# Kernel optimization log

Measured on AMD Instinct MI355X. Metric: run time of the kernel, lower is better.

Reference implementation:

```python
import jax, jax.numpy as jnp
import numpy as np

N = 50000      # nodes
E = 1600000    # edges (nnz of A)
D_IN = 512
D_H = 512
D_OUT = 40
L = 3
LN_EPS = 1e-5
BN_EPS = 1e-5


def setup_inputs() -> dict:
    key = jax.random.key(0)
    ks = jax.random.split(key, 10)
    x = jax.random.normal(ks[0], (N, D_IN), dtype=jnp.float32)
    edge_src = jax.random.randint(ks[1], (E,), 0, N, dtype=jnp.int32)
    edge_dst = jax.random.randint(ks[2], (E,), 0, N, dtype=jnp.int32)
    s = 1.0 / np.sqrt(D_IN)
    W_in = (jax.random.normal(ks[3], (D_IN, D_H), dtype=jnp.float32) * s)
    b_in = jnp.zeros((D_H,), jnp.float32)
    ln_g = jnp.ones((D_H,), jnp.float32)
    ln_b = jnp.zeros((D_H,), jnp.float32)
    cW1 = (jax.random.normal(ks[4], (D_H, D_H), dtype=jnp.float32) * s)
    cb1 = jnp.zeros((D_H,), jnp.float32)
    bn_g = 1.0 + 0.1 * jax.random.normal(ks[5], (D_H,), dtype=jnp.float32)
    bn_b = 0.1 * jax.random.normal(ks[6], (D_H,), dtype=jnp.float32)
    bn_mean = jnp.zeros((D_H,), jnp.float32)   # eval-mode running stats
    bn_var = jnp.ones((D_H,), jnp.float32)
    cW2 = (jax.random.normal(ks[7], (D_H, D_OUT), dtype=jnp.float32) * s)
    cb2 = jnp.zeros((D_OUT,), jnp.float32)
    return dict(x=x, edge_src=edge_src, edge_dst=edge_dst, W_in=W_in, b_in=b_in,
                ln_g=ln_g, ln_b=ln_b, cW1=cW1, cb1=cb1, bn_g=bn_g, bn_b=bn_b,
                bn_mean=bn_mean, bn_var=bn_var, cW2=cW2, cb2=cb2)


def _agg_angle(h, edge_src, edge_dst, dinv):
    # diag(D^-1/2 A D^-1/2 @ CosSim^T)[i] = sum_{(i,j) in A} dinv_i dinv_j cos(h_i,h_j)
    nrm = jnp.sqrt(jnp.sum(h * h, axis=1, keepdims=True))  # torch.norm p=2
    hn = h / (nrm + 1e-4)
    cos_e = jnp.clip(jnp.sum(hn[edge_src] * hn[edge_dst], axis=1), -1.0, 1.0)  # [E]
    w_e = dinv[edge_src] * dinv[edge_dst] * cos_e
    return jax.ops.segment_sum(w_e, edge_src, num_segments=N)  # [N]


def _forward(x, edge_src, edge_dst, W_in, b_in, ln_g, ln_b, cW1, cb1,
             bn_g, bn_b, bn_mean, bn_var, cW2, cb2):
    h = jax.nn.relu(x @ W_in + b_in)
    mu = jnp.mean(h, axis=-1, keepdims=True)
    var = jnp.var(h, axis=-1, keepdims=True)
    h = (h - mu) / jnp.sqrt(var + LN_EPS) * ln_g + ln_b   # LayerNorm
    # dropout: eval mode -> identity
    # degree normalization (adjacency values are all 1.0); constant across layers
    deg = jax.ops.segment_sum(jnp.ones((E,), h.dtype), edge_src, num_segments=N)
    dinv = jnp.where(deg > 0, deg ** -0.5, 0.0)
    for _ in range(L):
        ang = _agg_angle(h, edge_src, edge_dst, dinv)  # [N]
        c, s = jnp.cos(ang), jnp.sin(ang)
        r0 = c * h[:, 0] - s * h[:, 1]   # 2x2 Givens rotation on first two dims
        r1 = s * h[:, 0] + c * h[:, 1]
        h = jnp.concatenate([jnp.stack([r0, r1], axis=1), h[:, 2:]], axis=1)
    # classifier: Linear -> ReLU -> BatchNorm1d (eval) -> Linear
    z = jax.nn.relu(h @ cW1 + cb1)
    z = (z - bn_mean) / jnp.sqrt(bn_var + BN_EPS) * bn_g + bn_b
    logits = z @ cW2 + cb2
    return jax.nn.log_softmax(logits, axis=1)


def reference(x, edge_src, edge_dst, W_in, b_in, ln_g, ln_b, cW1, cb1,
              bn_g, bn_b, bn_mean, bn_var, cW2, cb2):
    return _forward(x, edge_src, edge_dst, W_in, b_in, ln_g, ln_b, cW1, cb1,
                    bn_g, bn_b, bn_mean, bn_var, cW2, cb2)
```

## Files before the change

kernel.cpp:

```cpp
#include <hip/hip_runtime.h>
#include <hip/hip_bf16.h>
#include <math.h>

typedef unsigned short u16;
typedef unsigned int u32;

#define N_NODES 50000
#define N_EDGES 1600000
#define DIM     512
#define DOUT    40
#define MPAD    50048
#define QROW    256
#define NBKT    196
#define NB1     256
#define CHUNK   6250

typedef __bf16 bf16x8 __attribute__((ext_vector_type(8)));
typedef float  f32x4  __attribute__((ext_vector_type(4)));

__device__ inline u16 f2bf(float f) {
    union { float f; u32 u; } v; v.f = f;
    u32 u = v.u;
    u32 r = u + 0x7fffu + ((u >> 16) & 1u);
    return (u16)(r >> 16);
}
__device__ inline float2 bfpair(u32 u) {
    float2 r;
    union { u32 i; float f; } lo, hi;
    lo.i = u << 16; hi.i = u & 0xffff0000u;
    r.x = lo.f; r.y = hi.f; return r;
}
__device__ inline float wave_sum(float v) {
    #pragma unroll
    for (int o = 32; o > 0; o >>= 1) v += __shfl_xor(v, o);
    return v;
}
__device__ inline float wave_max(float v) {
    #pragma unroll
    for (int o = 32; o > 0; o >>= 1) v = fmaxf(v, __shfl_xor(v, o));
    return v;
}
__device__ inline int wave_sum_i(int v) {
    #pragma unroll
    for (int o = 32; o > 0; o >>= 1) v += __shfl_xor(v, o);
    return v;
}
#if __has_builtin(__builtin_amdgcn_sdot8)
__device__ inline int dot8(int a, int b, int c) {
    return __builtin_amdgcn_sdot8(a, b, c, false);
}
#else
__device__ inline int dot8(int a, int b, int c) {
    #pragma unroll
    for (int j = 0; j < 8; ++j) {
        int av = ((int)((u32)a << (28 - 4 * j))) >> 28;
        int bv = ((int)((u32)b << (28 - 4 * j))) >> 28;
        c += av * bv;
    }
    return c;
}
#endif
__device__ inline void gload16(const void* g, void* l) {
    __builtin_amdgcn_global_load_lds((const __attribute__((address_space(1))) u32*)g,
                                     (__attribute__((address_space(3))) u32*)l, 16, 0, 0);
}
__device__ inline int block_incl_scan(int v, int tid) {
    int lane = tid & 63, w = tid >> 6;
    #pragma unroll
    for (int o = 1; o < 64; o <<= 1) {
        int t = __shfl_up(v, o);
        if (lane >= o) v += t;
    }
    __shared__ int wsum[4];
    if (lane == 63) wsum[w] = v;
    __syncthreads();
    if (w > 0) v += wsum[0];
    if (w > 1) v += wsum[1];
    if (w > 2) v += wsum[2];
    return v;
}

__global__ __launch_bounds__(256) void k_conv_x(const float* __restrict__ x,
                                                u16* __restrict__ xb) {
    long idx = (long)blockIdx.x * 256 + threadIdx.x;
    long base = idx * 4;
    if (base >= (long)MPAD * DIM) return;
    long row = base >> 9;
    float4 v;
    if (row < N_NODES) v = *(const float4*)(x + base);
    else { v.x = v.y = v.z = v.w = 0.f; }
    ushort4 o;
    o.x = f2bf(v.x); o.y = f2bf(v.y); o.z = f2bf(v.z); o.w = f2bf(v.w);
    *(ushort4*)(xb + base) = o;
}

__global__ __launch_bounds__(256) void k_transpose2(const float* __restrict__ W0,
                                                    const float* __restrict__ W1,
                                                    u16* __restrict__ T0,
                                                    u16* __restrict__ T1) {
    const float* W = blockIdx.z ? W1 : W0;
    u16* T = blockIdx.z ? T1 : T0;
    int n = blockIdx.x * 16 + threadIdx.x;
    int k = blockIdx.y * 16 + threadIdx.y;
    T[(long)n * 512 + k] = f2bf(W[(long)k * 512 + n]);
}
__global__ __launch_bounds__(256) void k_prep_w2(const float* __restrict__ cW2,
                                                 u16* __restrict__ W2b) {
    int idx = blockIdx.x * 256 + threadIdx.x;
    if (idx >= 48 * DIM) return;
    int n = idx >> 9;
    int k = idx & 511;
    float v = (n < DOUT) ? cW2[(long)k * DOUT + n] : 0.f;
    W2b[idx] = f2bf(v);
}

__global__ __launch_bounds__(256) void k_ms_count(const int* __restrict__ esrc,
                                                  int* __restrict__ C) {
    __shared__ int bcnt[NBKT];
    int tid = threadIdx.x, blk = blockIdx.x;
    if (tid < NBKT) bcnt[tid] = 0;
    __syncthreads();
    int e0 = blk * CHUNK, e1 = e0 + CHUNK;
    for (int e = e0 + tid; e < e1; e += 256)
        atomicAdd(&bcnt[esrc[e] >> 8], 1);
    __syncthreads();
    if (tid < NBKT) C[tid * NB1 + blk] = bcnt[tid];
}
__global__ __launch_bounds__(256) void k_ms_scan_partial(const int* __restrict__ C,
                                                         int* __restrict__ psum2) {
    int v = C[blockIdx.x * 256 + threadIdx.x];
    int t = wave_sum_i(v);
    __shared__ int ws[4];
    int lane = threadIdx.x & 63, w = threadIdx.x >> 6;
    if (lane == 0) ws[w] = t;
    __syncthreads();
    if (threadIdx.x == 0) psum2[blockIdx.x] = ws[0] + ws[1] + ws[2] + ws[3];
}
__global__ __launch_bounds__(256) void k_ms_scan_base(const int* __restrict__ psum2,
                                                      int* __restrict__ pb2) {
    int tid = threadIdx.x;
    int v = (tid < NBKT) ? psum2[tid] : 0;
    int incl = block_incl_scan(v, tid);
    if (tid < NBKT) pb2[tid] = incl - v;
}
__global__ __launch_bounds__(256) void k_ms_scan_add(const int* __restrict__ C,
                                                     const int* __restrict__ pb2,
                                                     int* __restrict__ O) {
    int idx = blockIdx.x * 256 + threadIdx.x;
    int v = C[idx];
    int incl = block_incl_scan(v, threadIdx.x);
    O[idx] = pb2[blockIdx.x] + incl - v;
}
__global__ __launch_bounds__(256) void k_ms_scatter(const int* __restrict__ esrc,
                                                    const int* __restrict__ edst,
                                                    const int* __restrict__ O,
                                                    uint2* __restrict__ tmp) {
    __shared__ int cur[NBKT];
    int tid = threadIdx.x, blk = blockIdx.x;
    if (tid < NBKT) cur[tid] = O[tid * NB1 + blk];
    __syncthreads();
    int e0 = blk * CHUNK, e1 = e0 + CHUNK;
    for (int e = e0 + tid; e < e1; e += 256) {
        int s = esrc[e], d = edst[e];
        int pos = atomicAdd(&cur[s >> 8], 1);
        uint2 pr; pr.x = (u32)s; pr.y = (u32)d;
        tmp[pos] = pr;
    }
}
__global__ __launch_bounds__(256) void k_bucket(const int* __restrict__ Om,
                                                const uint2* __restrict__ tmp,
                                                int* __restrict__ rowptr,
                                                float* __restrict__ dinv,
                                                int* __restrict__ edst_s) {
    __shared__ int cnt[256];
    __shared__ int curs[256];
    int tid = threadIdx.x, b = blockIdx.x;
    int base = b * 256;
    int start = Om[b * NB1];
    int end = (b == NBKT - 1) ? N_EDGES : Om[(b + 1) * NB1];
    cnt[tid] = 0;
    __syncthreads();
    for (int p = start + tid; p < end; p += 256)
        atomicAdd(&cnt[(int)tmp[p].x - base], 1);
    __syncthreads();
    int c = cnt[tid];
    int incl = block_incl_scan(c, tid);
    int excl = incl - c;
    int node = base + tid;
    if (node < N_NODES) {
        rowptr[node] = start + excl;
        dinv[node] = (c > 0) ? (1.f / sqrtf((float)c)) : 0.f;
    }
    if (b == NBKT - 1 && tid == 0) rowptr[N_NODES] = N_EDGES;
    curs[tid] = start + excl;
    __syncthreads();
    for (int p = start + tid; p < end; p += 256) {
        uint2 pr = tmp[p];
        int pos = atomicAdd(&curs[(int)pr.x - base], 1);
        edst_s[pos] = (int)pr.y;
    }
}

template<int EPI>
__global__ __launch_bounds__(256) void k_gemm(const u16* __restrict__ A,
                                              const u16* __restrict__ Bt,
                                              u16* __restrict__ outB,
                                              const float* __restrict__ bias,
                                              const float* __restrict__ bn_g,
                                              const float* __restrict__ bn_b,
                                              const float* __restrict__ bn_mean,
                                              const float* __restrict__ bn_var) {
    __shared__ u16 lds[2 * 128 * 64];
    char* ldsA = (char*)lds;
    char* ldsB = (char*)lds + 16384;

    const int bid = blockIdx.x;
    const int xcd = bid & 7;
    const int j = bid >> 3;
    const int tm = xcd * 49 + (j >> 2);
    const int tn = j & 3;
    if (tm >= MPAD / 128) return;

    const int tid = threadIdx.x;
    const int l = tid & 63, wid = tid >> 6;
    const int wr = wid >> 1, wc = wid & 1;
    const int lm = l & 15, lk = l >> 4;

    const int srow = tid >> 3;
    const int kq   = tid & 7;

    f32x4 acc[4][4] = {};

    for (int kt = 0; kt < 8; ++kt) {
        const int k0 = kt * 64;
        #pragma unroll
        for (int r = 0; r < 4; ++r) {
            int row = r * 32 + srow;
            int kc = (kq ^ (row & 7)) * 8;
            const u16* ga = A + ((long)tm * 128 + row) * DIM + k0 + kc;
            const u16* gb = Bt + ((long)tn * 128 + row) * DIM + k0 + kc;
            char* la = ldsA + r * 4096 + wid * 1024;
            char* lb = ldsB + r * 4096 + wid * 1024;
            gload16(ga, la);
            gload16(gb, lb);
        }
        __syncthreads();
        #pragma unroll
        for (int kk = 0; kk < 2; ++kk) {
            bf16x8 af[4], bfr[4];
            #pragma unroll
            for (int m = 0; m < 4; ++m) {
                int ar = wr * 64 + m * 16 + lm;
                af[m] = *(const bf16x8*)(ldsA + ar * 128 + ((kk * 64 + lk * 16) ^ ((ar & 7) << 4)));
            }
            #pragma unroll
            for (int n = 0; n < 4; ++n) {
                int br = wc * 64 + n * 16 + lm;
                bfr[n] = *(const bf16x8*)(ldsB + br * 128 + ((kk * 64 + lk * 16) ^ ((br & 7) << 4)));
            }
            #pragma unroll
            for (int m = 0; m < 4; ++m)
                #pragma unroll
                for (int n = 0; n < 4; ++n)
                    acc[m][n] = __builtin_amdgcn_mfma_f32_16x16x32_bf16(af[m], bfr[n], acc[m][n], 0, 0, 0);
        }
        __syncthreads();
    }

    #pragma unroll
    for (int n = 0; n < 4; ++n) {
        int col = tn * 128 + wc * 64 + n * 16 + lm;
        float bc = bias[col];
        float scale = 0.f, shift = 0.f;
        if (EPI == 1) {
            scale = bn_g[col] / sqrtf(bn_var[col] + 1e-5f);
            shift = bn_b[col] - bn_mean[col] * scale;
        }
        #pragma unroll
        for (int m = 0; m < 4; ++m) {
            f32x4 v = acc[m][n];
            #pragma unroll
            for (int r = 0; r < 4; ++r) {
                long row = (long)tm * 128 + wr * 64 + m * 16 + lk * 4 + r;
                float val = fmaxf(v[r] + bc, 0.f);
                if (EPI == 1) val = val * scale + shift;
                outB[row * DIM + col] = f2bf(val);
            }
        }
    }
}

__global__ __launch_bounds__(256) void k_ln(u16* __restrict__ hb,
                                            char* __restrict__ hq,
                                            float* __restrict__ stepr,
                                            const float* __restrict__ g,
                                            const float* __restrict__ b,
                                            float* __restrict__ a0,
                                            float* __restrict__ a1,
                                            float* __restrict__ inv_nrm) {
    int row = blockIdx.x * 4 + (threadIdx.x >> 6);
    int l = threadIdx.x & 63;
    u16* prow = hb + (long)row * DIM + l * 8;
    if (row >= N_NODES) {
        if (row < MPAD) { uint4 z; z.x = z.y = z.z = z.w = 0u; *(uint4*)prow = z; }
        return;
    }
    uint4 v = *(const uint4*)prow;
    float x[8];
    { float2 p;
      p = bfpair(v.x); x[0] = p.x; x[1] = p.y;
      p = bfpair(v.y); x[2] = p.x; x[3] = p.y;
      p = bfpair(v.z); x[4] = p.x; x[5] = p.y;
      p = bfpair(v.w); x[6] = p.x; x[7] = p.y; }
    float s = 0.f, sq = 0.f;
    #pragma unroll
    for (int j = 0; j < 8; ++j) { s += x[j]; sq += x[j] * x[j]; }
    #pragma unroll
    for (int o = 32; o > 0; o >>= 1) { s += __shfl_xor(s, o); sq += __shfl_xor(sq, o); }
    float mean = s * (1.f / DIM);
    float var = sq * (1.f / DIM) - mean * mean;
    float rstd = 1.f / sqrtf(var + 1e-5f);
    float y[8];
    #pragma unroll
    for (int j = 0; j < 8; ++j) {
        int c = l * 8 + j;
        y[j] = (x[j] - mean) * rstd * g[c] + b[c];
    }
    float s2 = 0.f;
    #pragma unroll
    for (int j = 0; j < 8; ++j) s2 += y[j] * y[j];
    s2 = wave_sum(s2);
    float nrm = sqrtf(s2);
    float inv = 1.f / (nrm + 1e-4f);
    ushort4 oh;
    oh.x = f2bf(y[0]); oh.y = f2bf(y[1]); oh.z = f2bf(y[2]); oh.w = f2bf(y[3]);
    *(ushort4*)prow = oh;
    oh.x = f2bf(y[4]); oh.y = f2bf(y[5]); oh.z = f2bf(y[6]); oh.w = f2bf(y[7]);
    *(ushort4*)(prow + 4) = oh;
    float nv[8];
    float mx = 0.f;
    #pragma unroll
    for (int j = 0; j < 8; ++j) { nv[j] = y[j] * inv; mx = fmaxf(mx, fabsf(nv[j])); }
    mx = wave_max(mx);
    float qs = (mx > 0.f) ? (7.f / mx) : 0.f;
    if (l == 0) { nv[0] = 0.f; nv[1] = 0.f; }
    u32 w = 0;
    #pragma unroll
    for (int j = 0; j < 8; ++j) {
        int q = (int)rintf(nv[j] * qs);
        w |= ((u32)(q & 0xF)) << (4 * j);
    }
    *(u32*)(hq + (long)row * QROW + l * 4) = w;
    if (l == 0) {
        stepr[row] = (mx > 0.f) ? (mx * (1.f / 7.f)) : 0.f;
        a0[row] = y[0]; a1[row] = y[1]; inv_nrm[row] = inv;
    }
}

__global__ __launch_bounds__(256) void k_edge_dot(const int* __restrict__ rowptr,
                                                  const int* __restrict__ edst_s,
                                                  const char* __restrict__ hq,
                                                  const float* __restrict__ stepr,
                                                  float* __restrict__ rest) {
    int node = blockIdx.x * 4 + (threadIdx.x >> 6);
    if (node >= N_NODES) return;
    int l = threadIdx.x & 63;
    int le = l & 7;
    int eg = l >> 3;
    int p0 = rowptr[node], p1 = rowptr[node + 1];
    if (p0 == p1) return;
    const int4* srow = (const int4*)(hq + (long)node * QROW);
    int4 s0 = srow[le * 2], s1 = srow[le * 2 + 1];
    float ss = stepr[node];
    #pragma unroll 2
    for (int base = p0; base < p1; base += 8) {
        int p = base + eg;
        bool ok = p < p1;
        int d = ok ? edst_s[p] : 0;
        const int4* drow = (const int4*)(hq + (long)d * QROW);
        int4 d0 = drow[le * 2], d1 = drow[le * 2 + 1];
        int acc = 0;
        acc = dot8(s0.x, d0.x, acc); acc = dot8(s0.y, d0.y, acc);
        acc = dot8(s0.z, d0.z, acc); acc = dot8(s0.w, d0.w, acc);
        acc = dot8(s1.x, d1.x, acc); acc = dot8(s1.y, d1.y, acc);
        acc = dot8(s1.z, d1.z, acc); acc = dot8(s1.w, d1.w, acc);
        acc += __shfl_xor(acc, 4);
        acc += __shfl_xor(acc, 2);
        acc += __shfl_xor(acc, 1);
        if (ok && le == 0) rest[p] = ss * stepr[d] * (float)acc;
    }
}

template<int WRITE_HB>
__global__ __launch_bounds__(256) void k_layer(const int* __restrict__ rowptr,
                                               const int* __restrict__ edst_s,
                                               const float* __restrict__ rest,
                                               const float* __restrict__ a0i,
                                               const float* __restrict__ a1i,
                                               const float* __restrict__ invn,
                                               const float* __restrict__ dinv,
                                               float* __restrict__ a0o,
                                               float* __restrict__ a1o,
                                               u16* __restrict__ hb) {
    int node = blockIdx.x * 4 + (threadIdx.x >> 6);
    if (node >= N_NODES) return;
    int l = threadIdx.x & 63;
    int p0 = rowptr[node], p1 = rowptr[node + 1];
    float x = a0i[node], y = a1i[node];
    float si = invn[node];
    float sa0 = x * si, sa1 = y * si;
    float accum = 0.f;
    for (int p = p0 + l; p < p1; p += 64) {
        int d = edst_s[p];
        float c = rest[p] + (sa0 * a0i[d] + sa1 * a1i[d]) * invn[d];
        c = fminf(1.f, fmaxf(-1.f, c));
        accum += dinv[d] * c;
    }
    accum = wave_sum(accum);
    if (l == 0) {
        float ang = dinv[node] * accum;
        float sn, cs;
        sincosf(ang, &sn, &cs);
        float r0 = cs * x - sn * y;
        float r1 = sn * x + cs * y;
        a0o[node] = r0;
        a1o[node] = r1;
        if (WRITE_HB) {
            hb[(long)node * DIM + 0] = f2bf(r0);
            hb[(long)node * DIM + 1] = f2bf(r1);
        }
    }
}

__global__ __launch_bounds__(256) void k_final(const u16* __restrict__ zb,
                                               const u16* __restrict__ W2b,
                                               const float* __restrict__ cb2,
                                               float* __restrict__ out) {
    __shared__ char ldsB[48 * 1024];
    const int tid = threadIdx.x;
    #pragma unroll
    for (int i = 0; i < 12; ++i) {
        int unit = i * 256 + tid;
        int byte = unit * 16;
        int row = byte >> 10;
        int colb = byte & 1023;
        uint4 v = *(const uint4*)((const char*)W2b + byte);
        *(uint4*)(ldsB + row * 1024 + (colb ^ ((row & 7) << 4))) = v;
    }
    __syncthreads();

    const int l = tid & 63, wid = tid >> 6;
    const int lm = l & 15, lk = l >> 4;
    const long m0 = (long)blockIdx.x * 128 + wid * 32;

    f32x4 acc[2][3] = {};
    for (int kt = 0; kt < 16; ++kt) {
        const int k0 = kt * 32;
        bf16x8 af[2], bfr[3];
        #pragma unroll
        for (int m = 0; m < 2; ++m)
            af[m] = *(const bf16x8*)(zb + (m0 + m * 16 + lm) * DIM + k0 + lk * 8);
        #pragma unroll
        for (int n = 0; n < 3; ++n) {
            int br = n * 16 + lm;
            bfr[n] = *(const bf16x8*)(ldsB + br * 1024 + ((k0 * 2 + lk * 16) ^ ((br & 7) << 4)));
        }
        #pragma unroll
        for (int m = 0; m < 2; ++m)
            #pragma unroll
            for (int n = 0; n < 3; ++n)
                acc[m][n] = __builtin_amdgcn_mfma_f32_16x16x32_bf16(af[m], bfr[n], acc[m][n], 0, 0, 0);
    }

    float bc[3];
    #pragma unroll
    for (int n = 0; n < 3; ++n) {
        int col = n * 16 + lm;
        bc[n] = (col < DOUT) ? cb2[col] : 0.f;
    }

    #pragma unroll
    for (int m = 0; m < 2; ++m) {
        #pragma unroll
        for (int r = 0; r < 4; ++r) {
            long row = m0 + m * 16 + lk * 4 + r;
            float v[3];
            float mv = -1e30f;
            #pragma unroll
            for (int n = 0; n < 3; ++n) {
                int col = n * 16 + lm;
                float t = (col < DOUT) ? (acc[m][n][r] + bc[n]) : -1e30f;
                v[n] = t;
                mv = fmaxf(mv, t);
            }
            #pragma unroll
            for (int o = 8; o > 0; o >>= 1) mv = fmaxf(mv, __shfl_xor(mv, o));
            float es = 0.f;
            #pragma unroll
            for (int n = 0; n < 3; ++n) {
                int col = n * 16 + lm;
                if (col < DOUT) es += expf(v[n] - mv);
            }
            #pragma unroll
            for (int o = 8; o > 0; o >>= 1) es += __shfl_xor(es, o);
            float lse = logf(es);
            if (row < N_NODES) {
                #pragma unroll
                for (int n = 0; n < 3; ++n) {
                    int col = n * 16 + lm;
                    if (col < DOUT) out[row * DOUT + col] = v[n] - mv - lse;
                }
            }
        }
    }
}

extern "C" void kernel_launch(void* const* d_in, const int* in_sizes, int n_in,
                              void* d_out, int out_size, void* d_ws, size_t ws_size,
                              hipStream_t stream) {
    const float* x       = (const float*)d_in[0];
    const int*   esrc    = (const int*)d_in[1];
    const int*   edst    = (const int*)d_in[2];
    const float* W_in    = (const float*)d_in[3];
    const float* b_in    = (const float*)d_in[4];
    const float* ln_g    = (const float*)d_in[5];
    const float* ln_b    = (const float*)d_in[6];
    const float* cW1     = (const float*)d_in[7];
    const float* cb1     = (const float*)d_in[8];
    const float* bn_g    = (const float*)d_in[9];
    const float* bn_b    = (const float*)d_in[10];
    const float* bn_mean = (const float*)d_in[11];
    const float* bn_var  = (const float*)d_in[12];
    const float* cW2     = (const float*)d_in[13];
    const float* cb2     = (const float*)d_in[14];
    float* out = (float*)d_out;

    char* ws = (char*)d_ws;
    size_t off = 0;
    auto take = [&](size_t bytes) -> char* {
        char* p = ws + off;
        off = (off + bytes + 255) & ~(size_t)255;
        return p;
    };
    u16*   xb     = (u16*)take((size_t)MPAD * DIM * 2);
    u16*   hb     = (u16*)take((size_t)MPAD * DIM * 2);
    char*  hq     = (char*)take((size_t)N_NODES * QROW);
    float* stepr  = (float*)take((size_t)N_NODES * 4);
    u16*   WtIn   = (u16*)take((size_t)512 * 512 * 2);
    u16*   W1t    = (u16*)take((size_t)512 * 512 * 2);
    u16*   W2b    = (u16*)take((size_t)48 * 512 * 2);
    float* dinv   = (float*)take((size_t)N_NODES * 4);
    float* a0A    = (float*)take((size_t)N_NODES * 4);
    float* a1A    = (float*)take((size_t)N_NODES * 4);
    float* a0B    = (float*)take((size_t)N_NODES * 4);
    float* a1B    = (float*)take((size_t)N_NODES * 4);
    float* invn   = (float*)take((size_t)N_NODES * 4);
    float* rest   = (float*)take((size_t)N_EDGES * 4);
    int*   rowptr = (int*)take((size_t)(N_NODES + 1) * 4);
    int*   edst_s = (int*)take((size_t)N_EDGES * 4);
    uint2* tmp    = (uint2*)take((size_t)N_EDGES * 8);
    int*   Cm     = (int*)take((size_t)NBKT * NB1 * 4);
    int*   Om     = (int*)take((size_t)NBKT * NB1 * 4);
    int*   psum2  = (int*)take((size_t)NBKT * 4);
    int*   pb2    = (int*)take((size_t)NBKT * 4);
    u16*   zb     = xb;

    k_conv_x<<<(MPAD * DIM / 4 + 255) / 256, 256, 0, stream>>>(x, xb);
    k_transpose2<<<dim3(32, 32, 2), dim3(16, 16), 0, stream>>>(W_in, cW1, WtIn, W1t);
    k_prep_w2<<<(48 * DIM + 255) / 256, 256, 0, stream>>>(cW2, W2b);

    k_ms_count<<<NB1, 256, 0, stream>>>(esrc, Cm);
    k_ms_scan_partial<<<NBKT, 256, 0, stream>>>(Cm, psum2);
    k_ms_scan_base<<<1, 256, 0, stream>>>(psum2, pb2);
    k_ms_scan_add<<<NBKT, 256, 0, stream>>>(Cm, pb2, Om);
    k_ms_scatter<<<NB1, 256, 0, stream>>>(esrc, edst, Om, tmp);
    k_bucket<<<NBKT, 256, 0, stream>>>(Om, tmp, rowptr, dinv, edst_s);

    k_gemm<0><<<1568, 256, 0, stream>>>(xb, WtIn, hb, b_in,
                                        nullptr, nullptr, nullptr, nullptr);
    k_ln<<<MPAD / 4, 256, 0, stream>>>(hb, hq, stepr, ln_g, ln_b, a0A, a1A, invn);
    k_edge_dot<<<(N_NODES + 3) / 4, 256, 0, stream>>>(rowptr, edst_s, hq, stepr, rest);

    k_layer<0><<<(N_NODES + 3) / 4, 256, 0, stream>>>(rowptr, edst_s, rest,
                                                      a0A, a1A, invn, dinv, a0B, a1B, nullptr);
    k_layer<0><<<(N_NODES + 3) / 4, 256, 0, stream>>>(rowptr, edst_s, rest,
                                                      a0B, a1B, invn, dinv, a0A, a1A, nullptr);
    k_layer<1><<<(N_NODES + 3) / 4, 256, 0, stream>>>(rowptr, edst_s, rest,
                                                      a0A, a1A, invn, dinv, a0B, a1B, hb);

    k_gemm<1><<<1568, 256, 0, stream>>>(hb, W1t, zb, cb1,
                                        bn_g, bn_b, bn_mean, bn_var);
    k_final<<<MPAD / 128, 256, 0, stream>>>(zb, W2b, cb2, out);
}
```

Measured before the change: 363.5 us.

## Fuse first rotation layer into edge-dot, pack bucket pairs, merge weight prep kernels

The first Givens-rotation layer is folded into the edge-dot kernel: as each edge's quantized residual dot is computed, the kernel also forms the clipped cosine and accumulates the angle, then applies the rotation. This removes one full pass over the CSR edges and a kernel launch. The edge-sort scratch buffer is packed from 8-byte (src,dst) pairs into 4-byte words holding the local source index and destination, halving scatter/bucket traffic. Destinations are stored in 16 bits, so node ids of 65536 or more would overflow; with 50000 nodes they fit. The two weight-prep kernels are merged into one launch, and the unroll factor of the edge loop is raised.

```diff
diff --git a/kernel.cpp b/kernel.cpp
--- a/kernel.cpp
+++ b/kernel.cpp
@@ -94,24 +94,28 @@
     *(ushort4*)(xb + base) = o;
 }
 
-__global__ __launch_bounds__(256) void k_transpose2(const float* __restrict__ W0,
-                                                    const float* __restrict__ W1,
-                                                    u16* __restrict__ T0,
-                                                    u16* __restrict__ T1) {
-    const float* W = blockIdx.z ? W1 : W0;
-    u16* T = blockIdx.z ? T1 : T0;
-    int n = blockIdx.x * 16 + threadIdx.x;
-    int k = blockIdx.y * 16 + threadIdx.y;
-    T[(long)n * 512 + k] = f2bf(W[(long)k * 512 + n]);
-}
-__global__ __launch_bounds__(256) void k_prep_w2(const float* __restrict__ cW2,
-                                                 u16* __restrict__ W2b) {
-    int idx = blockIdx.x * 256 + threadIdx.x;
-    if (idx >= 48 * DIM) return;
-    int n = idx >> 9;
-    int k = idx & 511;
-    float v = (n < DOUT) ? cW2[(long)k * DOUT + n] : 0.f;
-    W2b[idx] = f2bf(v);
+__global__ __launch_bounds__(256) void k_prep(const float* __restrict__ W_in,
+                                              const float* __restrict__ cW1,
+                                              const float* __restrict__ cW2,
+                                              u16* __restrict__ WtIn,
+                                              u16* __restrict__ W1t,
+                                              u16* __restrict__ W2b) {
+    int z = blockIdx.z;
+    if (z < 2) {
+        const float* W = z ? cW1 : W_in;
+        u16* T = z ? W1t : WtIn;
+        int n = blockIdx.x * 16 + threadIdx.x;
+        int k = blockIdx.y * 16 + threadIdx.y;
+        T[(long)n * 512 + k] = f2bf(W[(long)k * 512 + n]);
+    } else {
+        int idx = (blockIdx.y * 32 + blockIdx.x) * 256 + threadIdx.y * 16 + threadIdx.x;
+        if (idx < 48 * DIM) {
+            int n = idx >> 9;
+            int k = idx & 511;
+            float v = (n < DOUT) ? cW2[(long)k * DOUT + n] : 0.f;
+            W2b[idx] = f2bf(v);
+        }
+    }
 }
 
 __global__ __launch_bounds__(256) void k_ms_count(const int* __restrict__ esrc,
@@ -154,7 +158,7 @@
 __global__ __launch_bounds__(256) void k_ms_scatter(const int* __restrict__ esrc,
                                                     const int* __restrict__ edst,
                                                     const int* __restrict__ O,
-                                                    uint2* __restrict__ tmp) {
+                                                    u32* __restrict__ pk) {
     __shared__ int cur[NBKT];
     int tid = threadIdx.x, blk = blockIdx.x;
     if (tid < NBKT) cur[tid] = O[tid * NB1 + blk];
@@ -163,12 +167,11 @@
     for (int e = e0 + tid; e < e1; e += 256) {
         int s = esrc[e], d = edst[e];
         int pos = atomicAdd(&cur[s >> 8], 1);
-        uint2 pr; pr.x = (u32)s; pr.y = (u32)d;
-        tmp[pos] = pr;
+        pk[pos] = ((u32)(s & 255) << 16) | (u32)d;
     }
 }
 __global__ __launch_bounds__(256) void k_bucket(const int* __restrict__ Om,
-                                                const uint2* __restrict__ tmp,
+                                                const u32* __restrict__ pk,
                                                 int* __restrict__ rowptr,
                                                 float* __restrict__ dinv,
                                                 int* __restrict__ edst_s) {
@@ -181,7 +184,7 @@
     cnt[tid] = 0;
     __syncthreads();
     for (int p = start + tid; p < end; p += 256)
-        atomicAdd(&cnt[(int)tmp[p].x - base], 1);
+        atomicAdd(&cnt[pk[p] >> 16], 1);
     __syncthreads();
     int c = cnt[tid];
     int incl = block_incl_scan(c, tid);
@@ -195,9 +198,9 @@
     curs[tid] = start + excl;
     __syncthreads();
     for (int p = start + tid; p < end; p += 256) {
-        uint2 pr = tmp[p];
-        int pos = atomicAdd(&curs[(int)pr.x - base], 1);
-        edst_s[pos] = (int)pr.y;
+        u32 pr = pk[p];
+        int pos = atomicAdd(&curs[pr >> 16], 1);
+        edst_s[pos] = (int)(pr & 0xFFFFu);
     }
 }
 
@@ -361,18 +364,31 @@
                                                   const int* __restrict__ edst_s,
                                                   const char* __restrict__ hq,
                                                   const float* __restrict__ stepr,
-                                                  float* __restrict__ rest) {
+                                                  const float* __restrict__ a0i,
+                                                  const float* __restrict__ a1i,
+                                                  const float* __restrict__ invn,
+                                                  const float* __restrict__ dinv,
+                                                  float* __restrict__ rest,
+                                                  float* __restrict__ a0o,
+                                                  float* __restrict__ a1o) {
     int node = blockIdx.x * 4 + (threadIdx.x >> 6);
     if (node >= N_NODES) return;
     int l = threadIdx.x & 63;
     int le = l & 7;
     int eg = l >> 3;
     int p0 = rowptr[node], p1 = rowptr[node + 1];
-    if (p0 == p1) return;
+    float xa = a0i[node], ya = a1i[node];
+    if (p0 == p1) {
+        if (l == 0) { a0o[node] = xa; a1o[node] = ya; }
+        return;
+    }
     const int4* srow = (const int4*)(hq + (long)node * QROW);
     int4 s0 = srow[le * 2], s1 = srow[le * 2 + 1];
     float ss = stepr[node];
-    #pragma unroll 2
+    float si = invn[node];
+    float sa0 = xa * si, sa1 = ya * si;
+    float accum = 0.f;
+    #pragma unroll 4
     for (int base = p0; base < p1; base += 8) {
         int p = base + eg;
         bool ok = p < p1;
@@ -387,7 +403,21 @@
         acc += __shfl_xor(acc, 4);
         acc += __shfl_xor(acc, 2);
         acc += __shfl_xor(acc, 1);
-        if (ok && le == 0) rest[p] = ss * stepr[d] * (float)acc;
+        if (ok && le == 0) {
+            float r = ss * stepr[d] * (float)acc;
+            rest[p] = r;
+            float c = r + (sa0 * a0i[d] + sa1 * a1i[d]) * invn[d];
+            c = fminf(1.f, fmaxf(-1.f, c));
+            accum += dinv[d] * c;
+        }
+    }
+    accum = wave_sum(accum);
+    if (l == 0) {
+        float ang = dinv[node] * accum;
+        float sn, cs;
+        sincosf(ang, &sn, &cs);
+        a0o[node] = cs * xa - sn * ya;
+        a1o[node] = sn * xa + cs * ya;
     }
 }
 
@@ -558,7 +588,7 @@
     float* rest   = (float*)take((size_t)N_EDGES * 4);
     int*   rowptr = (int*)take((size_t)(N_NODES + 1) * 4);
     int*   edst_s = (int*)take((size_t)N_EDGES * 4);
-    uint2* tmp    = (uint2*)take((size_t)N_EDGES * 8);
+    u32*   pk     = (u32*)take((size_t)N_EDGES * 4);
     int*   Cm     = (int*)take((size_t)NBKT * NB1 * 4);
     int*   Om     = (int*)take((size_t)NBKT * NB1 * 4);
     int*   psum2  = (int*)take((size_t)NBKT * 4);
@@ -566,23 +596,20 @@
     u16*   zb     = xb;
 
     k_conv_x<<<(MPAD * DIM / 4 + 255) / 256, 256, 0, stream>>>(x, xb);
-    k_transpose2<<<dim3(32, 32, 2), dim3(16, 16), 0, stream>>>(W_in, cW1, WtIn, W1t);
-    k_prep_w2<<<(48 * DIM + 255) / 256, 256, 0, stream>>>(cW2, W2b);
+    k_prep<<<dim3(32, 32, 3), dim3(16, 16), 0, stream>>>(W_in, cW1, cW2, WtIn, W1t, W2b);
 
     k_ms_count<<<NB1, 256, 0, stream>>>(esrc, Cm);
     k_ms_scan_partial<<<NBKT, 256, 0, stream>>>(Cm, psum2);
     k_ms_scan_base<<<1, 256, 0, stream>>>(psum2, pb2);
     k_ms_scan_add<<<NBKT, 256, 0, stream>>>(Cm, pb2, Om);
-    k_ms_scatter<<<NB1, 256, 0, stream>>>(esrc, edst, Om, tmp);
-    k_bucket<<<NBKT, 256, 0, stream>>>(Om, tmp, rowptr, dinv, edst_s);
+    k_ms_scatter<<<NB1, 256, 0, stream>>>(esrc, edst, Om, pk);
+    k_bucket<<<NBKT, 256, 0, stream>>>(Om, pk, rowptr, dinv, edst_s);
 
     k_gemm<0><<<1568, 256, 0, stream>>>(xb, WtIn, hb, b_in,
                                         nullptr, nullptr, nullptr, nullptr);
     k_ln<<<MPAD / 4, 256, 0, stream>>>(hb, hq, stepr, ln_g, ln_b, a0A, a1A, invn);
-    k_edge_dot<<<(N_NODES + 3) / 4, 256, 0, stream>>>(rowptr, edst_s, hq, stepr, rest);
-
-    k_layer<0><<<(N_NODES + 3) / 4, 256, 0, stream>>>(rowptr, edst_s, rest,
-                                                      a0A, a1A, invn, dinv, a0B, a1B, nullptr);
+    k_edge_dot<<<(N_NODES + 3) / 4, 256, 0, stream>>>(rowptr, edst_s, hq, stepr,
+                                                      a0A, a1A, invn, dinv, rest, a0B, a1B);
     k_layer<0><<<(N_NODES + 3) / 4, 256, 0, stream>>>(rowptr, edst_s, rest,
                                                       a0B, a1B, invn, dinv, a0A, a1A, nullptr);
     k_layer<1><<<(N_NODES + 3) / 4, 256, 0, stream>>>(rowptr, edst_s, rest,
```

Result: faster. 343.0 us (-5.7%).
